# Optimization experiments

Hardware: AMD Instinct MI355X
Metric: run time of the kernel (lower is better)

The kernel has to match this reference:

```python
import jax, jax.numpy as jnp
import numpy as np

N = 16000
E = 128000
IN_DIM = 512
H1 = 4096
H2 = 1024
OUT_DIM = 64


def setup_inputs() -> dict:
    key = jax.random.key(0)
    ks = jax.random.split(key, 8)
    x = jax.random.normal(ks[0], (N, IN_DIM), dtype=jnp.float32)
    edge_index = jax.random.randint(ks[1], (2, E), 0, N, dtype=jnp.int64)

    def glorot(k, fan_in, fan_out):
        lim = float(np.sqrt(6.0 / (fan_in + fan_out)))
        return jax.random.uniform(k, (fan_in, fan_out), jnp.float32, -lim, lim)

    # PyG SAGEConv: out = lin_l(mean_j x_j) + lin_r(x); lin_l has bias, lin_r does not.
    params = {
        'W1l': glorot(ks[2], IN_DIM, H1), 'b1': jnp.zeros((H1,), jnp.float32),
        'W1r': glorot(ks[3], IN_DIM, H1),
        'W2l': glorot(ks[4], H1, H2), 'b2': jnp.zeros((H2,), jnp.float32),
        'W2r': glorot(ks[5], H1, H2),
        'W3l': glorot(ks[6], H2, OUT_DIM), 'b3': jnp.zeros((OUT_DIM,), jnp.float32),
        'W3r': glorot(ks[7], H2, OUT_DIM),
    }
    return {'x': x, 'edge_index': edge_index, **params}


def _sage_conv(x, src, dst, Wl, b, Wr):
    # mean-aggregate neighbor features at dst, then linear; plus root transform
    agg = jax.ops.segment_sum(x[src], dst, num_segments=N)          # [N, F_in]
    cnt = jax.ops.segment_sum(jnp.ones((src.shape[0],), x.dtype), dst, num_segments=N)
    mean = agg / jnp.maximum(cnt, 1.0)[:, None]
    return mean @ Wl + b + x @ Wr


def reference(x, edge_index, W1l, b1, W1r, W2l, b2, W2r, W3l, b3, W3r):
    src, dst = edge_index[0], edge_index[1]
    h = jax.nn.relu(_sage_conv(x, src, dst, W1l, b1, W1r))   # dropout is identity in eval
    h = jax.nn.relu(_sage_conv(h, src, dst, W2l, b2, W2r))
    h = _sage_conv(h, src, dst, W3l, b3, W3r)
    return jax.nn.log_softmax(h, axis=1)
```

## Files before the change

### kernel.cpp

```cpp
#include <hip/hip_runtime.h>
#include <stdint.h>

typedef __bf16 bf16x8 __attribute__((ext_vector_type(8)));
typedef float  f32x4  __attribute__((ext_vector_type(4)));
typedef const void __attribute__((address_space(1))) gv_t;
typedef void __attribute__((address_space(3))) sv_t;

static __device__ __forceinline__ unsigned short f2bf(float f) {
  unsigned u = __float_as_uint(f);
  u += 0x7fffu + ((u >> 16) & 1u);
  return (unsigned short)(u >> 16);
}
static __device__ __forceinline__ float bf2f(unsigned short h) {
  return __uint_as_float(((unsigned)h) << 16);
}
static __device__ __forceinline__ void gload16(const void* g, void* l) {
  __builtin_amdgcn_global_load_lds((gv_t*)g, (sv_t*)l, 16, 0, 0);
}

__global__ void k_sentinel(float* out, int n, float val) {
  int t = blockIdx.x * 256 + threadIdx.x;
  if (t < n) out[t] = val;
}
__global__ void k_zero(int* p, int n) {
  int t = blockIdx.x * 256 + threadIdx.x;
  if (t < n) p[t] = 0;
}

__global__ void k_detect(const int* ei, int* flag) {
  if (blockIdx.x == 0 && threadIdx.x == 0) {
    int nz = 0;
    for (int t = 0; t < 256; ++t) nz += (ei[2 * t + 1] != 0);
    *flag = (nz == 0) ? 1 : 0;
  }
}

__global__ void k_degree(const int* ei, int E, const int* flag, int* deg) {
  int t = blockIdx.x * 256 + threadIdx.x;
  if (t < E) {
    int d = (*flag) ? ei[2 * (E + t)] : ei[E + t];
    atomicAdd(&deg[d], 1);
  }
}
__global__ void k_scan(const int* deg, int* rp, int* cur, int n) {
  __shared__ int ssum[256];
  int t = threadIdx.x;
  int chunk = (n + 255) >> 8;
  int lo = t * chunk, hi = min(lo + chunk, n);
  int s = 0;
  for (int i = lo; i < hi; ++i) s += deg[i];
  ssum[t] = s;
  __syncthreads();
  if (t == 0) {
    int run = 0;
    for (int i = 0; i < 256; ++i) { int v = ssum[i]; ssum[i] = run; run += v; }
  }
  __syncthreads();
  int run = ssum[t];
  for (int i = lo; i < hi; ++i) { rp[i] = run; cur[i] = run; run += deg[i]; }
  if (t == 255) rp[n] = run;
}
__global__ void k_fill(const int* ei, int E, const int* flag, int* cur, int* col) {
  int t = blockIdx.x * 256 + threadIdx.x;
  if (t < E) {
    int f = *flag;
    int s = f ? ei[2 * t] : ei[t];
    int d = f ? ei[2 * (E + t)] : ei[E + t];
    int p = atomicAdd(&cur[d], 1);
    col[p] = s;
  }
}

__global__ void k_cvtx(const float4* __restrict__ in, ushort4* __restrict__ xm, int total4) {
  int t = blockIdx.x * 256 + threadIdx.x;
  if (t < total4) {
    int row = t >> 7, c = t & 127;
    float4 v = in[t];
    xm[(size_t)row * 256 + c] = make_ushort4(f2bf(v.x), f2bf(v.y), f2bf(v.z), f2bf(v.w));
  }
}

__global__ void k_transW(const float* W, unsigned short* Wt, int K, int N, int ld, int kofs) {
  __shared__ float tile[32][33];
  int tx = threadIdx.x & 31, ty = threadIdx.x >> 5;
  int n0 = blockIdx.x << 5, k0 = blockIdx.y << 5;
#pragma unroll
  for (int r = 0; r < 4; ++r)
    tile[ty + r * 8][tx] = W[(size_t)(k0 + ty + r * 8) * N + n0 + tx];
  __syncthreads();
#pragma unroll
  for (int r = 0; r < 4; ++r)
    Wt[(size_t)(n0 + ty + r * 8) * ld + kofs + k0 + tx] = f2bf(tile[tx][ty + r * 8]);
}

__global__ void k_agg(ushort4* __restrict__ xm, const int* __restrict__ rp,
                      const int* __restrict__ col) {
  int i = blockIdx.x;
  int s = rp[i], e = rp[i + 1];
  float inv = 1.0f / (float)max(e - s, 1);
  int f = threadIdx.x;
  float4 a = make_float4(0.f, 0.f, 0.f, 0.f);
  for (int n = s; n < e; ++n) {
    ushort4 v = xm[(size_t)col[n] * 256 + f];
    a.x += bf2f(v.x); a.y += bf2f(v.y); a.z += bf2f(v.z); a.w += bf2f(v.w);
  }
  xm[(size_t)i * 256 + 128 + f] =
      make_ushort4(f2bf(a.x * inv), f2bf(a.y * inv), f2bf(a.z * inv), f2bf(a.w * inv));
}

template <bool RELU, bool BIAS>
__global__ __launch_bounds__(512, 1) void k_gemm256(
    const unsigned short* __restrict__ A, const unsigned short* __restrict__ B,
    const float* __restrict__ bias, unsigned short* __restrict__ outp,
    int Mreal, int N, int K, int bnShift) {
  __shared__ __align__(16) unsigned short lds[2][2][256 * 64];

  const int tid = threadIdx.x;
  const int lane = tid & 63;
  const int wq = tid >> 6;
  const int wr = wq >> 2;
  const int wc = wq & 3;

  const int nwg = gridDim.x;
  const int q8 = nwg >> 3, r8 = nwg & 7;
  const int xcd = blockIdx.x & 7, idx = blockIdx.x >> 3;
  const int wg = (xcd < r8 ? xcd * (q8 + 1) : r8 * (q8 + 1) + (xcd - r8) * q8) + idx;
  const int bn = wg & ((1 << bnShift) - 1);
  const int bm = wg >> bnShift;

  const unsigned short* Ap = A + (size_t)bm * 256 * K;
  const unsigned short* Bp = B + (size_t)bn * 256 * K;
  const int sl8 = ((lane & 7) ^ (lane >> 3)) * 8;
  const int rsub = wq * 8 + (lane >> 3);

#define STAGE_A(BUF, I, K0)                                            \
  gload16(Ap + (size_t)((I) * 64 + rsub) * K + (K0) + sl8,             \
          (char*)&lds[BUF][0][0] + ((I) * 64 + wq * 8) * 128)
#define STAGE_B(BUF, I, K0)                                            \
  gload16(Bp + (size_t)((I) * 64 + rsub) * K + (K0) + sl8,             \
          (char*)&lds[BUF][1][0] + ((I) * 64 + wq * 8) * 128)

  f32x4 acc[8][4];
#pragma unroll
  for (int m = 0; m < 8; ++m)
#pragma unroll
    for (int n = 0; n < 4; ++n) acc[m][n] = (f32x4){0.f, 0.f, 0.f, 0.f};

#define LOAD_AFR(DST, CUR, QA)                                                          \
  do {                                                                                  \
    const char* baseA = (const char*)&lds[CUR][0][0];                                   \
    _Pragma("unroll") for (int mm = 0; mm < 4; ++mm) {                                  \
      const int rr = ((QA) * 4 + mm) * 32 + wr * 16 + (lane & 15);                      \
      _Pragma("unroll") for (int kk = 0; kk < 2; ++kk)                                  \
          DST[mm][kk] = *(const bf16x8*)(baseA + rr * 128 +                             \
                                         (((kk * 4 + (lane >> 4)) ^ (lane & 7)) << 4)); \
    }                                                                                   \
  } while (0)
#define LOAD_BFR(DST, CUR, QB)                                                          \
  do {                                                                                  \
    const char* baseB = (const char*)&lds[CUR][1][0];                                   \
    _Pragma("unroll") for (int nn = 0; nn < 2; ++nn) {                                  \
      const int cc = ((QB) * 2 + nn) * 64 + wc * 16 + (lane & 15);                      \
      _Pragma("unroll") for (int kk = 0; kk < 2; ++kk)                                  \
          DST[nn][kk] = *(const bf16x8*)(baseB + cc * 128 +                             \
                                         (((kk * 4 + (lane >> 4)) ^ (lane & 7)) << 4)); \
    }                                                                                   \
  } while (0)
#define MFMA_Q(QA, QB, AFR, BFR)                                                        \
  do {                                                                                  \
    _Pragma("unroll") for (int mm = 0; mm < 4; ++mm)                                    \
        _Pragma("unroll") for (int nn = 0; nn < 2; ++nn)                                \
            _Pragma("unroll") for (int kk = 0; kk < 2; ++kk)                            \
                acc[(QA) * 4 + mm][(QB) * 2 + nn] =                                     \
                    __builtin_amdgcn_mfma_f32_16x16x32_bf16(                            \
                        AFR[mm][kk], BFR[nn][kk], acc[(QA) * 4 + mm][(QB) * 2 + nn],    \
                        0, 0, 0);                                                       \
  } while (0)

  STAGE_A(0, 0, 0); STAGE_A(0, 1, 0);
  STAGE_B(0, 0, 0); STAGE_B(0, 1, 0);
  STAGE_B(0, 2, 0); STAGE_B(0, 3, 0);
  STAGE_A(0, 2, 0); STAGE_A(0, 3, 0);
  STAGE_A(1, 0, 64); STAGE_A(1, 1, 64);
  STAGE_B(1, 0, 64); STAGE_B(1, 1, 64);
  STAGE_B(1, 2, 64); STAGE_B(1, 3, 64);
  STAGE_A(1, 2, 64); STAGE_A(1, 3, 64);
  asm volatile("s_waitcnt vmcnt(8)" ::: "memory");
  __builtin_amdgcn_s_barrier();

  bf16x8 a0[4][2], b0[2][2], a1[4][2], b1[2][2];
  LOAD_AFR(a0, 0, 0);
  LOAD_BFR(b0, 0, 0);

  const int nt = K >> 6;
#pragma unroll 1
  for (int t = 0; t < nt; ++t) {
    const int cur = t & 1, nxt = cur ^ 1;
    const int k2 = (t + 2) << 6;
    LOAD_AFR(a1, cur, 1);
    LOAD_BFR(b1, cur, 1);
    __builtin_amdgcn_s_setprio(1);
    MFMA_Q(0, 0, a0, b0);
    MFMA_Q(0, 1, a0, b1);
    __builtin_amdgcn_s_setprio(0);
    asm volatile("s_waitcnt vmcnt(0) lgkmcnt(0)" ::: "memory");
    __builtin_amdgcn_s_barrier();
    if (t + 2 < nt) {
      STAGE_A(cur, 0, k2); STAGE_A(cur, 1, k2);
      STAGE_B(cur, 0, k2); STAGE_B(cur, 1, k2);
      STAGE_B(cur, 2, k2); STAGE_B(cur, 3, k2);
      STAGE_A(cur, 2, k2); STAGE_A(cur, 3, k2);
    }
    __builtin_amdgcn_s_setprio(1);
    MFMA_Q(1, 0, a1, b0);
    MFMA_Q(1, 1, a1, b1);
    __builtin_amdgcn_s_setprio(0);
    if (t + 1 < nt) {
      LOAD_AFR(a0, nxt, 0);
      LOAD_BFR(b0, nxt, 0);
    }
  }

  const int row0 = bm * 256 + wr * 16 + ((lane >> 4) << 2);
  const int col0 = bn * 256 + wc * 16 + (lane & 15);
#pragma unroll
  for (int m = 0; m < 8; ++m) {
#pragma unroll
    for (int n = 0; n < 4; ++n) {
      const int col = col0 + n * 64;
      float bb = BIAS ? bias[col] : 0.f;
#pragma unroll
      for (int r = 0; r < 4; ++r) {
        int row = row0 + m * 32 + r;
        if (row < Mreal) {
          float v = acc[m][n][r] + bb;
          if (RELU) v = fmaxf(v, 0.f);
          outp[(size_t)row * N + col] = f2bf(v);
        }
      }
    }
  }
#undef MFMA_Q
#undef LOAD_BFR
#undef LOAD_AFR
#undef STAGE_A
#undef STAGE_B
}

template <int NF, bool TWO, bool RELU, bool BIAS>
__global__ __launch_bounds__(256) void k_gemm(
    const unsigned short* __restrict__ Am, const unsigned short* __restrict__ Ar,
    const unsigned short* __restrict__ Bl, const unsigned short* __restrict__ Br,
    const float* __restrict__ bias, unsigned short* __restrict__ outp, int N, int K) {
  constexpr int BN = NF * 32;
  __shared__ __align__(16) unsigned short lds[(128 + BN) * 64];
  unsigned short* ldsA = lds;
  unsigned short* ldsB = lds + 128 * 64;

  const int tid = threadIdx.x;
  const int lane = tid & 63;
  const int w = tid >> 6;
  const int wr = w >> 1, wc = w & 1;

  f32x4 zero = {0.f, 0.f, 0.f, 0.f};
  f32x4 acc[4][NF];
#pragma unroll
  for (int m = 0; m < 4; ++m)
#pragma unroll
    for (int n = 0; n < NF; ++n) acc[m][n] = zero;

  const int bm = blockIdx.x, bn = blockIdx.y;
  const int sl_st = (lane & 7) ^ (lane >> 3);

#pragma unroll 1
  for (int pass = 0; pass < (TWO ? 2 : 1); ++pass) {
    const unsigned short* A = (TWO && pass) ? Ar : Am;
    const unsigned short* B = (TWO && pass) ? Br : Bl;
    A += (size_t)bm * 128 * K;
    B += (size_t)bn * BN * K;
#pragma unroll 1
    for (int k0 = 0; k0 < K; k0 += 64) {
      __syncthreads();
#pragma unroll
      for (int q = 0; q < 4; ++q) {
        int rowi = (w * 4 + q) * 8 + (lane >> 3);
        gload16(A + (size_t)rowi * K + k0 + sl_st * 8, (char*)ldsA + (w * 4 + q) * 1024);
      }
#pragma unroll
      for (int q = 0; q < NF; ++q) {
        int rowi = (w * NF + q) * 8 + (lane >> 3);
        gload16(B + (size_t)rowi * K + k0 + sl_st * 8, (char*)ldsB + (w * NF + q) * 1024);
      }
      __syncthreads();
#pragma unroll
      for (int kk = 0; kk < 2; ++kk) {
        int sw = (((kk * 4 + (lane >> 4)) ^ (lane & 7)) << 4);
        bf16x8 af[4], bfr[NF];
#pragma unroll
        for (int m = 0; m < 4; ++m) {
          int r = wr * 64 + m * 16 + (lane & 15);
          af[m] = *(const bf16x8*)((const char*)ldsA + r * 128 + sw);
        }
#pragma unroll
        for (int n = 0; n < NF; ++n) {
          int c = wc * (BN / 2) + n * 16 + (lane & 15);
          bfr[n] = *(const bf16x8*)((const char*)ldsB + c * 128 + sw);
        }
#pragma unroll
        for (int m = 0; m < 4; ++m)
#pragma unroll
          for (int n = 0; n < NF; ++n)
            acc[m][n] = __builtin_amdgcn_mfma_f32_16x16x32_bf16(af[m], bfr[n], acc[m][n], 0, 0, 0);
      }
    }
  }

  const int row0 = bm * 128 + wr * 64;
  const int col0 = bn * BN + wc * (BN / 2);
#pragma unroll
  for (int m = 0; m < 4; ++m) {
#pragma unroll
    for (int n = 0; n < NF; ++n) {
      int col = col0 + n * 16 + (lane & 15);
      float bb = BIAS ? bias[col] : 0.f;
#pragma unroll
      for (int r = 0; r < 4; ++r) {
        int row = row0 + m * 16 + ((lane >> 4) << 2) + r;
        float v = acc[m][n][r] + bb;
        if (RELU) v = fmaxf(v, 0.f);
        outp[(size_t)row * N + col] = f2bf(v);
      }
    }
  }
}

__global__ void k_combine2(const ushort4* __restrict__ Z2, const int* __restrict__ rp,
                           const int* __restrict__ col, const float* __restrict__ bias,
                           ushort4* __restrict__ h2) {
  int i = blockIdx.x;
  int s = rp[i], e = rp[i + 1];
  float inv = 1.0f / (float)max(e - s, 1);
  int f = threadIdx.x;
  float4 a = make_float4(0.f, 0.f, 0.f, 0.f);
  float4 b = make_float4(0.f, 0.f, 0.f, 0.f);
  int n = s;
  for (; n + 1 < e; n += 2) {
    int j0 = col[n], j1 = col[n + 1];
    ushort4 v0 = Z2[(size_t)j0 * 512 + f];
    ushort4 v1 = Z2[(size_t)j1 * 512 + f];
    a.x += bf2f(v0.x); a.y += bf2f(v0.y); a.z += bf2f(v0.z); a.w += bf2f(v0.w);
    b.x += bf2f(v1.x); b.y += bf2f(v1.y); b.z += bf2f(v1.z); b.w += bf2f(v1.w);
  }
  if (n < e) {
    ushort4 v0 = Z2[(size_t)col[n] * 512 + f];
    a.x += bf2f(v0.x); a.y += bf2f(v0.y); a.z += bf2f(v0.z); a.w += bf2f(v0.w);
  }
  a.x += b.x; a.y += b.y; a.z += b.z; a.w += b.w;
  ushort4 r = Z2[(size_t)i * 512 + 256 + f];
  float4 b4 = ((const float4*)bias)[f];
  float o0 = fmaxf(a.x * inv + bf2f(r.x) + b4.x, 0.f);
  float o1 = fmaxf(a.y * inv + bf2f(r.y) + b4.y, 0.f);
  float o2 = fmaxf(a.z * inv + bf2f(r.z) + b4.z, 0.f);
  float o3 = fmaxf(a.w * inv + bf2f(r.w) + b4.w, 0.f);
  h2[(size_t)i * 256 + f] = make_ushort4(f2bf(o0), f2bf(o1), f2bf(o2), f2bf(o3));
}

__global__ void k_combine3(const unsigned short* __restrict__ Z3, const int* __restrict__ rp,
                           const int* __restrict__ col, const float* __restrict__ bias,
                           float* __restrict__ out) {
  int i = blockIdx.x * 4 + (threadIdx.x >> 6);
  int c = threadIdx.x & 63;
  int s = rp[i], e = rp[i + 1];
  float inv = 1.0f / (float)max(e - s, 1);
  float a = 0.f;
  for (int n = s; n < e; ++n) a += bf2f(Z3[(size_t)col[n] * 128 + c]);
  float v = a * inv + bf2f(Z3[(size_t)i * 128 + 64 + c]) + bias[c];
  float m = v;
#pragma unroll
  for (int o = 1; o < 64; o <<= 1) m = fmaxf(m, __shfl_xor(m, o, 64));
  float t = expf(v - m);
  float sum = t;
#pragma unroll
  for (int o = 1; o < 64; o <<= 1) sum += __shfl_xor(sum, o, 64);
  out[(size_t)i * 64 + c] = (v - m) - logf(sum);
}

extern "C" void kernel_launch(void* const* d_in, const int* in_sizes, int n_in,
                              void* d_out, int out_size, void* d_ws, size_t ws_size,
                              hipStream_t stream) {
  const float* x   = (const float*)d_in[0];
  const int*   ei  = (const int*)d_in[1];
  const float* W1l = (const float*)d_in[2];
  const float* b1  = (const float*)d_in[3];
  const float* W1r = (const float*)d_in[4];
  const float* W2l = (const float*)d_in[5];
  const float* b2  = (const float*)d_in[6];
  const float* W2r = (const float*)d_in[7];
  const float* W3l = (const float*)d_in[8];
  const float* b3  = (const float*)d_in[9];
  const float* W3r = (const float*)d_in[10];

  const int Nn = 16000;
  const int E = in_sizes[1] / 2;

  char* p = (char*)d_ws;
  auto carve = [&](size_t bytes) {
    char* r = p;
    p += (bytes + 255) & ~(size_t)255;
    return r;
  };
  int* deg    = (int*)carve((size_t)Nn * 4);
  int* rp     = (int*)carve((size_t)(Nn + 1) * 4);
  int* cur    = (int*)carve((size_t)Nn * 4);
  int* flag   = (int*)carve(4);
  int* colidx = (int*)carve((size_t)E * 4);
  unsigned short* Wb = (unsigned short*)carve((size_t)2048 * 4096 * 2);
  unsigned short* xm = (unsigned short*)carve((size_t)Nn * 1024 * 2);
  unsigned short* h1 = (unsigned short*)carve((size_t)Nn * 4096 * 2);
  unsigned short* Z2 = (unsigned short*)carve((size_t)Nn * 2048 * 2);
  unsigned short* Z3 = (unsigned short*)carve((size_t)Nn * 128 * 2);
  unsigned short* h2 = xm;

  size_t need = (size_t)(p - (char*)d_ws);
  if (ws_size < need) {
    k_sentinel<<<(out_size + 255) / 256, 256, 0, stream>>>((float*)d_out, out_size,
                                                           (float)(ws_size >> 20));
    return;
  }

  k_zero<<<(Nn + 255) / 256, 256, 0, stream>>>(deg, Nn);
  k_detect<<<1, 64, 0, stream>>>(ei, flag);
  k_degree<<<(E + 255) / 256, 256, 0, stream>>>(ei, E, flag, deg);
  k_scan<<<1, 256, 0, stream>>>(deg, rp, cur, Nn);
  k_fill<<<(E + 255) / 256, 256, 0, stream>>>(ei, E, flag, cur, colidx);

  k_cvtx<<<(Nn * 128 + 255) / 256, 256, 0, stream>>>((const float4*)x, (ushort4*)xm, Nn * 128);
  k_transW<<<dim3(4096 / 32, 512 / 32), 256, 0, stream>>>(W1r, Wb, 512, 4096, 1024, 0);
  k_transW<<<dim3(4096 / 32, 512 / 32), 256, 0, stream>>>(W1l, Wb, 512, 4096, 1024, 512);
  k_agg<<<Nn, 128, 0, stream>>>((ushort4*)xm, rp, colidx);
  k_gemm256<true, true><<<63 * 16, 512, 0, stream>>>(xm, Wb, b1, h1, Nn, 4096, 1024, 4);

  k_transW<<<dim3(1024 / 32, 4096 / 32), 256, 0, stream>>>(W2l, Wb, 4096, 1024, 4096, 0);
  k_transW<<<dim3(1024 / 32, 4096 / 32), 256, 0, stream>>>(W2r, Wb + (size_t)1024 * 4096, 4096,
                                                           1024, 4096, 0);
  k_gemm256<false, false><<<63 * 8, 512, 0, stream>>>(h1, Wb, nullptr, Z2, Nn, 2048, 4096, 3);
  k_combine2<<<Nn, 256, 0, stream>>>((const ushort4*)Z2, rp, colidx, b2, (ushort4*)h2);

  k_transW<<<dim3(64 / 32, 1024 / 32), 256, 0, stream>>>(W3l, Wb, 1024, 64, 1024, 0);
  k_transW<<<dim3(64 / 32, 1024 / 32), 256, 0, stream>>>(W3r, Wb + (size_t)64 * 1024, 1024, 64,
                                                         1024, 0);
  k_gemm<2, false, false, false><<<dim3(125, 2), 256, 0, stream>>>(h2, nullptr, Wb, nullptr,
                                                                   nullptr, Z3, 128, 1024);
  k_combine3<<<Nn / 4, 256, 0, stream>>>(Z3, rp, colidx, b3, (float*)d_out);

  (void)n_in; (void)out_size;
}
```

Baseline: 591.8 us.

## Merge small launches and vectorize neighbor aggregation with split-edge reduction

```diff
diff --git a/kernel.cpp b/kernel.cpp
--- a/kernel.cpp
+++ b/kernel.cpp
@@ -3,6 +3,7 @@
 
 typedef __bf16 bf16x8 __attribute__((ext_vector_type(8)));
 typedef float  f32x4  __attribute__((ext_vector_type(4)));
+typedef unsigned short u16x8 __attribute__((ext_vector_type(8)));
 typedef const void __attribute__((address_space(1))) gv_t;
 typedef void __attribute__((address_space(3))) sv_t;
 
@@ -22,16 +23,16 @@
   int t = blockIdx.x * 256 + threadIdx.x;
   if (t < n) out[t] = val;
 }
-__global__ void k_zero(int* p, int n) {
+
+__global__ void k_init(int* deg, int n, const int* ei, int* flag) {
   int t = blockIdx.x * 256 + threadIdx.x;
-  if (t < n) p[t] = 0;
-}
-
-__global__ void k_detect(const int* ei, int* flag) {
-  if (blockIdx.x == 0 && threadIdx.x == 0) {
-    int nz = 0;
-    for (int t = 0; t < 256; ++t) nz += (ei[2 * t + 1] != 0);
-    *flag = (nz == 0) ? 1 : 0;
+  if (t < n) deg[t] = 0;
+  if (blockIdx.x == 0 && threadIdx.x < 64) {
+    int bad = 0;
+#pragma unroll
+    for (int j = 0; j < 4; ++j) bad |= ei[2 * (threadIdx.x * 4 + j) + 1];
+    unsigned long long m = __ballot(bad != 0);
+    if (threadIdx.x == 0) *flag = (m == 0ull) ? 1 : 0;
   }
 }
 
@@ -80,7 +81,11 @@
   }
 }
 
-__global__ void k_transW(const float* W, unsigned short* Wt, int K, int N, int ld, int kofs) {
+__global__ void k_transW2(const float* Wa, const float* Wb, unsigned short* Wta,
+                          unsigned short* Wtb, int K, int N, int ld, int kofsa, int kofsb) {
+  const float* W = blockIdx.z ? Wb : Wa;
+  unsigned short* Wt = blockIdx.z ? Wtb : Wta;
+  const int kofs = blockIdx.z ? kofsb : kofsa;
   __shared__ float tile[32][33];
   int tx = threadIdx.x & 31, ty = threadIdx.x >> 5;
   int n0 = blockIdx.x << 5, k0 = blockIdx.y << 5;
@@ -93,44 +98,52 @@
     Wt[(size_t)(n0 + ty + r * 8) * ld + kofs + k0 + tx] = f2bf(tile[tx][ty + r * 8]);
 }
 
-__global__ void k_agg(ushort4* __restrict__ xm, const int* __restrict__ rp,
+__global__ void k_agg(unsigned short* __restrict__ xm, const int* __restrict__ rp,
                       const int* __restrict__ col) {
   int i = blockIdx.x;
   int s = rp[i], e = rp[i + 1];
   float inv = 1.0f / (float)max(e - s, 1);
-  int f = threadIdx.x;
-  float4 a = make_float4(0.f, 0.f, 0.f, 0.f);
-  for (int n = s; n < e; ++n) {
-    ushort4 v = xm[(size_t)col[n] * 256 + f];
-    a.x += bf2f(v.x); a.y += bf2f(v.y); a.z += bf2f(v.z); a.w += bf2f(v.w);
-  }
-  xm[(size_t)i * 256 + 128 + f] =
-      make_ushort4(f2bf(a.x * inv), f2bf(a.y * inv), f2bf(a.z * inv), f2bf(a.w * inv));
-}
-
-template <bool RELU, bool BIAS>
-__global__ __launch_bounds__(512, 1) void k_gemm256(
-    const unsigned short* __restrict__ A, const unsigned short* __restrict__ B,
-    const float* __restrict__ bias, unsigned short* __restrict__ outp,
-    int Mreal, int N, int K, int bnShift) {
-  __shared__ __align__(16) unsigned short lds[2][2][256 * 64];
-
-  const int tid = threadIdx.x;
-  const int lane = tid & 63;
-  const int wq = tid >> 6;
-  const int wr = wq >> 2;
-  const int wc = wq & 3;
-
-  const int nwg = gridDim.x;
-  const int q8 = nwg >> 3, r8 = nwg & 7;
-  const int xcd = blockIdx.x & 7, idx = blockIdx.x >> 3;
-  const int wg = (xcd < r8 ? xcd * (q8 + 1) : r8 * (q8 + 1) + (xcd - r8) * q8) + idx;
-  const int bn = wg & ((1 << bnShift) - 1);
-  const int bm = wg >> bnShift;
-
-  const unsigned short* Ap = A + (size_t)bm * 256 * K;
-  const unsigned short* Bp = B + (size_t)bn * 256 * K;
-  const int sl8 = ((lane & 7) ^ (lane >> 3)) * 8;
+  int f8 = threadIdx.x & 63;
+  int p = threadIdx.x >> 6;
+  const u16x8* xm8 = (const u16x8*)xm;
+  float acc[8] = {0.f, 0.f, 0.f, 0.f, 0.f, 0.f, 0.f, 0.f};
+  for (int n = s + p; n < e; n += 4) {
+    u16x8 v = xm8[(size_t)col[n] * 128 + f8];
+#pragma unroll
+    for (int j = 0; j < 8; ++j) acc[j] += bf2f(v[j]);
+  }
+  __shared__ float red[3][64][8];
+  if (p > 0) {
+#pragma unroll
+    for (int j = 0; j < 8; ++j) red[p - 1][f8][j] = acc[j];
+  }
+  __syncthreads();
+  if (p == 0) {
+    u16x8 o;
+#pragma unroll
+    for (int j = 0; j < 8; ++j) {
+      float v = (acc[j] + red[0][f8][j] + red[1][f8][j] + red[2][f8][j]) * inv;
+      o[j] = f2bf(v);
+    }
+    ((u16x8*)xm)[(size_t)i * 128 + 64 + f8] = o;
+  }
+}
+
+#define GEMM256_SETUP(A_, B_, bnShift_)                                               \
+  const int tid = threadIdx.x;                                                        \
+  const int lane = tid & 63;                                                          \
+  const int wq = tid >> 6;                                                            \
+  const int wr = wq >> 2;                                                             \
+  const int wc = wq & 3;                                                              \
+  const int nwg = gridDim.x;                                                          \
+  const int q8 = nwg >> 3, r8 = nwg & 7;                                              \
+  const int xcd = blockIdx.x & 7, idx = blockIdx.x >> 3;                              \
+  const int wg = (xcd < r8 ? xcd * (q8 + 1) : r8 * (q8 + 1) + (xcd - r8) * q8) + idx; \
+  const int bn = wg & ((1 << (bnShift_)) - 1);                                        \
+  const int bm = wg >> (bnShift_);                                                    \
+  const unsigned short* Ap = (A_) + (size_t)bm * 256 * K;                             \
+  const unsigned short* Bp = (B_) + (size_t)bn * 256 * K;                             \
+  const int sl8 = ((lane & 7) ^ (lane >> 3)) * 8;                                     \
   const int rsub = wq * 8 + (lane >> 3);
 
 #define STAGE_A(BUF, I, K0)                                            \
@@ -139,12 +152,7 @@
 #define STAGE_B(BUF, I, K0)                                            \
   gload16(Bp + (size_t)((I) * 64 + rsub) * K + (K0) + sl8,             \
           (char*)&lds[BUF][1][0] + ((I) * 64 + wq * 8) * 128)
-
-  f32x4 acc[8][4];
-#pragma unroll
-  for (int m = 0; m < 8; ++m)
-#pragma unroll
-    for (int n = 0; n < 4; ++n) acc[m][n] = (f32x4){0.f, 0.f, 0.f, 0.f};
+#define VMCNT(NUM) asm volatile("s_waitcnt vmcnt(" #NUM ")" ::: "memory")
 
 #define LOAD_AFR(DST, CUR, QA)                                                          \
   do {                                                                                  \
@@ -177,6 +185,20 @@
                         0, 0, 0);                                                       \
   } while (0)
 
+template <bool RELU, bool BIAS>
+__global__ __launch_bounds__(512, 1) void k_gemm256(
+    const unsigned short* __restrict__ A, const unsigned short* __restrict__ B,
+    const float* __restrict__ bias, unsigned short* __restrict__ outp,
+    int Mreal, int N, int K, int bnShift) {
+  __shared__ __align__(16) unsigned short lds[2][2][256 * 64];
+  GEMM256_SETUP(A, B, bnShift)
+
+  f32x4 acc[8][4];
+#pragma unroll
+  for (int m = 0; m < 8; ++m)
+#pragma unroll
+    for (int n = 0; n < 4; ++n) acc[m][n] = (f32x4){0.f, 0.f, 0.f, 0.f};
+
   STAGE_A(0, 0, 0); STAGE_A(0, 1, 0);
   STAGE_B(0, 0, 0); STAGE_B(0, 1, 0);
   STAGE_B(0, 2, 0); STAGE_B(0, 3, 0);
@@ -185,7 +207,7 @@
   STAGE_B(1, 0, 64); STAGE_B(1, 1, 64);
   STAGE_B(1, 2, 64); STAGE_B(1, 3, 64);
   STAGE_A(1, 2, 64); STAGE_A(1, 3, 64);
-  asm volatile("s_waitcnt vmcnt(8)" ::: "memory");
+  VMCNT(8);
   __builtin_amdgcn_s_barrier();
 
   bf16x8 a0[4][2], b0[2][2], a1[4][2], b1[2][2];
@@ -240,11 +262,6 @@
       }
     }
   }
-#undef MFMA_Q
-#undef LOAD_BFR
-#undef LOAD_AFR
-#undef STAGE_A
-#undef STAGE_B
 }
 
 template <int NF, bool TWO, bool RELU, bool BIAS>
@@ -334,35 +351,40 @@
   }
 }
 
-__global__ void k_combine2(const ushort4* __restrict__ Z2, const int* __restrict__ rp,
+__global__ void k_combine2(const unsigned short* __restrict__ Z2, const int* __restrict__ rp,
                            const int* __restrict__ col, const float* __restrict__ bias,
-                           ushort4* __restrict__ h2) {
+                           unsigned short* __restrict__ h2) {
   int i = blockIdx.x;
   int s = rp[i], e = rp[i + 1];
   float inv = 1.0f / (float)max(e - s, 1);
-  int f = threadIdx.x;
-  float4 a = make_float4(0.f, 0.f, 0.f, 0.f);
-  float4 b = make_float4(0.f, 0.f, 0.f, 0.f);
-  int n = s;
-  for (; n + 1 < e; n += 2) {
-    int j0 = col[n], j1 = col[n + 1];
-    ushort4 v0 = Z2[(size_t)j0 * 512 + f];
-    ushort4 v1 = Z2[(size_t)j1 * 512 + f];
-    a.x += bf2f(v0.x); a.y += bf2f(v0.y); a.z += bf2f(v0.z); a.w += bf2f(v0.w);
-    b.x += bf2f(v1.x); b.y += bf2f(v1.y); b.z += bf2f(v1.z); b.w += bf2f(v1.w);
-  }
-  if (n < e) {
-    ushort4 v0 = Z2[(size_t)col[n] * 512 + f];
-    a.x += bf2f(v0.x); a.y += bf2f(v0.y); a.z += bf2f(v0.z); a.w += bf2f(v0.w);
-  }
-  a.x += b.x; a.y += b.y; a.z += b.z; a.w += b.w;
-  ushort4 r = Z2[(size_t)i * 512 + 256 + f];
-  float4 b4 = ((const float4*)bias)[f];
-  float o0 = fmaxf(a.x * inv + bf2f(r.x) + b4.x, 0.f);
-  float o1 = fmaxf(a.y * inv + bf2f(r.y) + b4.y, 0.f);
-  float o2 = fmaxf(a.z * inv + bf2f(r.z) + b4.z, 0.f);
-  float o3 = fmaxf(a.w * inv + bf2f(r.w) + b4.w, 0.f);
-  h2[(size_t)i * 256 + f] = make_ushort4(f2bf(o0), f2bf(o1), f2bf(o2), f2bf(o3));
+  int f8 = threadIdx.x & 127;
+  int p = threadIdx.x >> 7;
+  const u16x8* Z28 = (const u16x8*)Z2;
+  float acc[8] = {0.f, 0.f, 0.f, 0.f, 0.f, 0.f, 0.f, 0.f};
+  for (int n = s + p; n < e; n += 2) {
+    u16x8 v = Z28[(size_t)col[n] * 256 + f8];
+#pragma unroll
+    for (int j = 0; j < 8; ++j) acc[j] += bf2f(v[j]);
+  }
+  __shared__ float red[128][8];
+  if (p == 1) {
+#pragma unroll
+    for (int j = 0; j < 8; ++j) red[f8][j] = acc[j];
+  }
+  __syncthreads();
+  if (p == 0) {
+    u16x8 r = Z28[(size_t)i * 256 + 128 + f8];
+    float4 b4a = ((const float4*)bias)[f8 * 2];
+    float4 b4b = ((const float4*)bias)[f8 * 2 + 1];
+    float bb[8] = {b4a.x, b4a.y, b4a.z, b4a.w, b4b.x, b4b.y, b4b.z, b4b.w};
+    u16x8 o;
+#pragma unroll
+    for (int j = 0; j < 8; ++j) {
+      float v = (acc[j] + red[f8][j]) * inv + bf2f(r[j]) + bb[j];
+      o[j] = f2bf(fmaxf(v, 0.f));
+    }
+    ((u16x8*)h2)[(size_t)i * 128 + f8] = o;
+  }
 }
 
 __global__ void k_combine3(const unsigned short* __restrict__ Z3, const int* __restrict__ rp,
@@ -428,27 +450,24 @@
     return;
   }
 
-  k_zero<<<(Nn + 255) / 256, 256, 0, stream>>>(deg, Nn);
-  k_detect<<<1, 64, 0, stream>>>(ei, flag);
+  k_init<<<(Nn + 255) / 256, 256, 0, stream>>>(deg, Nn, ei, flag);
   k_degree<<<(E + 255) / 256, 256, 0, stream>>>(ei, E, flag, deg);
   k_scan<<<1, 256, 0, stream>>>(deg, rp, cur, Nn);
   k_fill<<<(E + 255) / 256, 256, 0, stream>>>(ei, E, flag, cur, colidx);
 
   k_cvtx<<<(Nn * 128 + 255) / 256, 256, 0, stream>>>((const float4*)x, (ushort4*)xm, Nn * 128);
-  k_transW<<<dim3(4096 / 32, 512 / 32), 256, 0, stream>>>(W1r, Wb, 512, 4096, 1024, 0);
-  k_transW<<<dim3(4096 / 32, 512 / 32), 256, 0, stream>>>(W1l, Wb, 512, 4096, 1024, 512);
-  k_agg<<<Nn, 128, 0, stream>>>((ushort4*)xm, rp, colidx);
+  k_transW2<<<dim3(4096 / 32, 512 / 32, 2), 256, 0, stream>>>(W1r, W1l, Wb, Wb, 512, 4096,
+                                                              1024, 0, 512);
+  k_agg<<<Nn, 256, 0, stream>>>(xm, rp, colidx);
   k_gemm256<true, true><<<63 * 16, 512, 0, stream>>>(xm, Wb, b1, h1, Nn, 4096, 1024, 4);
 
-  k_transW<<<dim3(1024 / 32, 4096 / 32), 256, 0, stream>>>(W2l, Wb, 4096, 1024, 4096, 0);
-  k_transW<<<dim3(1024 / 32, 4096 / 32), 256, 0, stream>>>(W2r, Wb + (size_t)1024 * 4096, 4096,
-                                                           1024, 4096, 0);
+  k_transW2<<<dim3(1024 / 32, 4096 / 32, 2), 256, 0, stream>>>(
+      W2l, W2r, Wb, Wb + (size_t)1024 * 4096, 4096, 1024, 4096, 0, 0);
   k_gemm256<false, false><<<63 * 8, 512, 0, stream>>>(h1, Wb, nullptr, Z2, Nn, 2048, 4096, 3);
-  k_combine2<<<Nn, 256, 0, stream>>>((const ushort4*)Z2, rp, colidx, b2, (ushort4*)h2);
-
-  k_transW<<<dim3(64 / 32, 1024 / 32), 256, 0, stream>>>(W3l, Wb, 1024, 64, 1024, 0);
-  k_transW<<<dim3(64 / 32, 1024 / 32), 256, 0, stream>>>(W3r, Wb + (size_t)64 * 1024, 1024, 64,
-                                                         1024, 0);
+  k_combine2<<<Nn, 256, 0, stream>>>(Z2, rp, colidx, b2, h2);
+
+  k_transW2<<<dim3(64 / 32, 1024 / 32, 2), 256, 0, stream>>>(
+      W3l, W3r, Wb, Wb + (size_t)64 * 1024, 1024, 64, 1024, 0, 0);
   k_gemm<2, false, false, false><<<dim3(125, 2), 256, 0, stream>>>(h2, nullptr, Wb, nullptr,
                                                                    nullptr, Z3, 128, 1024);
   k_combine3<<<Nn / 4, 256, 0, stream>>>(Z3, rp, colidx, b3, (float*)d_out);
```

Result: faster. 566.1 us (-4.3%).
